# Kernel optimization log

Measured on AMD Instinct MI355X. Metric: run time of the kernel, lower is better.

Reference implementation:

```python
import jax, jax.numpy as jnp
import numpy as np

MAX_DISP = 48
B, C, H, W = 2, 32, 128, 240


def setup_inputs() -> dict:
    key = jax.random.key(0)
    k1, k2 = jax.random.split(key)
    l_fmap = jax.random.normal(k1, (B, C, H, W), dtype=jnp.float32)
    r_fmap = jax.random.normal(k2, (B, C, H, W), dtype=jnp.float32)
    return {"l_fmap": l_fmap, "r_fmap": r_fmap}


def reference(l_fmap, r_fmap):
    # Output: [B, C, D, H, W] where out[..., d, :, w] =
    #   l[..., w] - r[..., w-d]  if w >= d else 1.0 (pad value)
    D = MAX_DISP
    Wdim = l_fmap.shape[-1]
    w = jnp.arange(Wdim)                       # [W]
    d = jnp.arange(D)[:, None]                 # [D,1]
    shift_idx = jnp.maximum(w[None, :] - d, 0) # [D,W], clamped gather index
    # Gather shifted right features: [B,C,H,W] indexed on last axis by [D,W] -> [B,C,H,D,W]
    r_shifted = r_fmap[..., shift_idx]
    r_shifted = jnp.transpose(r_shifted, (0, 1, 3, 2, 4))  # [B,C,D,H,W]
    diff = l_fmap[:, :, None, :, :] - r_shifted            # [B,C,D,H,W]
    valid = (w[None, :] >= d)                              # [D,W]
    cost_volume = jnp.where(valid[None, None, :, None, :], diff,
                            jnp.float32(1.0))
    return cost_volume
```

## Files before the change

kernel.cpp:

```cpp
#include <hip/hip_runtime.h>


#define MAX_DISP 48
#define HH 128
#define WW 240
#define NV 60
#define PAD4 12
#define ROW4 (PAD4 + NV)
#define HG 16

typedef float f32x4 __attribute__((ext_vector_type(4)));

__global__ __launch_bounds__(960) void costvol_kernel(
    const f32x4* __restrict__ l4,
    const f32x4* __restrict__ r4,
    f32x4* __restrict__ out4)
{
    __shared__ f32x4 r_lds[HG * ROW4];

    const int bc  = blockIdx.x & 63;
    const int hg  = blockIdx.x >> 6;
    const int h0  = hg * HG;
    const int tid = threadIdx.x;
    const int hl  = tid / NV;
    const int v   = tid % NV;

    if (tid < HG * PAD4) {
        r_lds[(tid / PAD4) * ROW4 + (tid % PAD4)] = (f32x4){0.f, 0.f, 0.f, 0.f};
    }
    const size_t in_base = ((size_t)bc * HH + h0) * NV;
    r_lds[hl * ROW4 + PAD4 + v] = r4[in_base + tid];
    const f32x4 lv = l4[in_base + tid];
    __syncthreads();

    const int w0 = 4 * v;
    size_t ob = ((size_t)bc * MAX_DISP * HH + h0 + hl) * NV + v;
    const size_t dstride4 = (size_t)HH * NV;

    #pragma unroll
    for (int k = 0; k < MAX_DISP / 4; ++k) {
        const int d0 = 4 * k;
        const f32x4 A = r_lds[hl * ROW4 + PAD4 + v - k];
        const f32x4 B = r_lds[hl * ROW4 + PAD4 + v - k - 1];

        #pragma unroll
        for (int s = 0; s < 4; ++s) {
            f32x4 o;
            #pragma unroll
            for (int j = 0; j < 4; ++j) {
                const int src = j - s;
                float rv = (src >= 0) ? A[src] : B[4 + src];
                o[j] = (w0 + j >= d0 + s) ? (lv[j] - rv) : 1.0f;
            }
            __builtin_nontemporal_store(o, &out4[ob + (size_t)(d0 + s) * dstride4]);
        }
    }
}

extern "C" void kernel_launch(void* const* d_in, const int* in_sizes, int n_in,
                              void* d_out, int out_size, void* d_ws, size_t ws_size,
                              hipStream_t stream) {
    const f32x4* l4 = (const f32x4*)d_in[0];
    const f32x4* r4 = (const f32x4*)d_in[1];
    f32x4* out4 = (f32x4*)d_out;

    const int nblocks = 64 * (HH / HG);
    costvol_kernel<<<nblocks, 960, 0, stream>>>(l4, r4, out4);
}
```

Before: 79.56 us.

## Assign one block per (bc, disparity) slab and read shifted right features from global

Restructures the grid so each 256-thread block writes one contiguous [H,W] output slab for a single batch-channel and disparity, instead of 960-thread blocks covering 16 rows across all disparities. The shared-memory staging and barrier are removed. Right-feature windows are loaded straight from global memory, with the sub-vector shift chosen by a template specialised on the disparity modulo 4. This is meant to make each block's store stream contiguous and to raise the block count for better occupancy. In exchange, the left and right inputs are re-read 48 times, relying on caches to absorb that traffic.

```diff
diff --git a/kernel.cpp b/kernel.cpp
--- a/kernel.cpp
+++ b/kernel.cpp
@@ -3,57 +3,60 @@
 
 #define MAX_DISP 48
 #define HH 128
-#define WW 240
 #define NV 60
-#define PAD4 12
-#define ROW4 (PAD4 + NV)
-#define HG 16
+#define SLAB (HH * NV)
 
 typedef float f32x4 __attribute__((ext_vector_type(4)));
 
-__global__ __launch_bounds__(960) void costvol_kernel(
+template <int M>
+__device__ __forceinline__ void slab_loop(
+    const f32x4* __restrict__ l4, const f32x4* __restrict__ r4,
+    f32x4* __restrict__ out4, size_t inbase, size_t obase, int d)
+{
+    for (int i = threadIdx.x; i < SLAB; i += 256) {
+        const int h  = i / NV;
+        const int v  = i - h * NV;
+        const int w0 = 4 * v;
+        const f32x4 lv = l4[inbase + i];
+
+        const int idx = w0 - d;
+        const int q   = idx >> 2;
+        const size_t rrow = inbase + (size_t)h * NV;
+        f32x4 A = (q >= 0) ? r4[rrow + q] : (f32x4){0.f, 0.f, 0.f, 0.f};
+        const int qb = (q + 1 < NV - 1) ? q + 1 : NV - 1;
+        f32x4 B = (q + 1 >= 0) ? r4[rrow + qb] : (f32x4){0.f, 0.f, 0.f, 0.f};
+
+        f32x4 win;
+        #pragma unroll
+        for (int t = 0; t < 4; ++t)
+            win[t] = (M + t < 4) ? A[M + t] : B[M + t - 4];
+
+        f32x4 o;
+        #pragma unroll
+        for (int j = 0; j < 4; ++j)
+            o[j] = (w0 + j >= d) ? (lv[j] - win[j]) : 1.0f;
+
+        __builtin_nontemporal_store(o, &out4[obase + i]);
+    }
+}
+
+__global__ __launch_bounds__(256) void costvol_kernel(
     const f32x4* __restrict__ l4,
     const f32x4* __restrict__ r4,
     f32x4* __restrict__ out4)
 {
-    __shared__ f32x4 r_lds[HG * ROW4];
+    const int blk = blockIdx.x;
+    const int d   = blk % MAX_DISP;
+    const int bc  = blk / MAX_DISP;
 
-    const int bc  = blockIdx.x & 63;
-    const int hg  = blockIdx.x >> 6;
-    const int h0  = hg * HG;
-    const int tid = threadIdx.x;
-    const int hl  = tid / NV;
-    const int v   = tid % NV;
+    const size_t inbase = (size_t)bc * SLAB;
+    const size_t obase  = (size_t)blk * SLAB;
 
-    if (tid < HG * PAD4) {
-        r_lds[(tid / PAD4) * ROW4 + (tid % PAD4)] = (f32x4){0.f, 0.f, 0.f, 0.f};
-    }
-    const size_t in_base = ((size_t)bc * HH + h0) * NV;
-    r_lds[hl * ROW4 + PAD4 + v] = r4[in_base + tid];
-    const f32x4 lv = l4[in_base + tid];
-    __syncthreads();
-
-    const int w0 = 4 * v;
-    size_t ob = ((size_t)bc * MAX_DISP * HH + h0 + hl) * NV + v;
-    const size_t dstride4 = (size_t)HH * NV;
-
-    #pragma unroll
-    for (int k = 0; k < MAX_DISP / 4; ++k) {
-        const int d0 = 4 * k;
-        const f32x4 A = r_lds[hl * ROW4 + PAD4 + v - k];
-        const f32x4 B = r_lds[hl * ROW4 + PAD4 + v - k - 1];
-
-        #pragma unroll
-        for (int s = 0; s < 4; ++s) {
-            f32x4 o;
-            #pragma unroll
-            for (int j = 0; j < 4; ++j) {
-                const int src = j - s;
-                float rv = (src >= 0) ? A[src] : B[4 + src];
-                o[j] = (w0 + j >= d0 + s) ? (lv[j] - rv) : 1.0f;
-            }
-            __builtin_nontemporal_store(o, &out4[ob + (size_t)(d0 + s) * dstride4]);
-        }
+    switch ((-d) & 3) {
+        case 0: slab_loop<0>(l4, r4, out4, inbase, obase, d); break;
+        case 1: slab_loop<1>(l4, r4, out4, inbase, obase, d); break;
+        case 2: slab_loop<2>(l4, r4, out4, inbase, obase, d); break;
+        case 3: slab_loop<3>(l4, r4, out4, inbase, obase, d); break;
     }
 }
 
@@ -64,6 +67,6 @@
     const f32x4* r4 = (const f32x4*)d_in[1];
     f32x4* out4 = (f32x4*)d_out;
 
-    const int nblocks = 64 * (HH / HG);
-    costvol_kernel<<<nblocks, 960, 0, stream>>>(l4, r4, out4);
+    const int nblocks = 64 * MAX_DISP;
+    costvol_kernel<<<nblocks, 256, 0, stream>>>(l4, r4, out4);
 }
```

Result: no change. 80.01 us (+0.6%).
